# Optimization experiments

Measured on AMD Instinct MI355X. Metric: run time of the kernel, lower is better.

## Reference

```python
import jax, jax.numpy as jnp
import numpy as np

H, NH, NL, FF, W, CMAX, V, L, G = 768, 12, 6, 3072, 256, 32, 50272, 4096, 64
DH = H // NH
SCALE = 1.0 / np.sqrt(DH)

def _ln(x, s, b, eps=1e-5):
    m = jnp.mean(x, -1, keepdims=True)
    v = jnp.mean((x - m) ** 2, -1, keepdims=True)
    return (x - m) * jax.lax.rsqrt(v + eps) * s + b

def _heads(x, B, Lx):
    return x.reshape(B, Lx, NH, DH).transpose(0, 2, 1, 3)  # [B,NH,L,DH]

def _layer(x, p, am, gpos, is_glob):
    (Wq, bq, Wk, bk, Wv, bv, Wqg, bqg, Wkg, bkg, Wvg, bvg, Wo, bo,
     ln1s, ln1b, W1, b1, W2, b2, ln2s, ln2b) = p
    B, Lx, _ = x.shape
    Nb = Lx // W
    q = _heads(x @ Wq + bq, B, Lx)
    k = _heads(x @ Wk + bk, B, Lx)
    v = _heads(x @ Wv + bv, B, Lx)
    qb = q.reshape(B, NH, Nb, W, DH)
    def ctx(t):  # gather 3 adjacent key/value blocks per query block
        tb = t.reshape(B, NH, Nb, W, DH)
        tp = jnp.pad(tb, ((0, 0), (0, 0), (1, 1), (0, 0), (0, 0)))
        return jnp.stack([tp[:, :, i:i + Nb] for i in range(3)], axis=3).reshape(B, NH, Nb, 3 * W, DH)
    k_ctx, v_ctx = ctx(k), ctx(v)
    s_loc = jnp.einsum('bhnqd,bhnkd->bhnqk', qb, k_ctx) * SCALE  # [B,NH,Nb,W,3W]
    rel = jnp.arange(3 * W)[None, :] - W - jnp.arange(W)[:, None]  # [W,3W]
    band = jnp.abs(rel) <= W
    pos = jnp.arange(Nb)[:, None] * W + jnp.arange(3 * W)[None, :] - W  # abs key pos [Nb,3W]
    inb = (pos >= 0) & (pos < Lx)
    safe = jnp.clip(pos, 0, Lx - 1)
    key_ok = inb & (~is_glob[safe]) & am[:, safe]  # [B,Nb,3W]; global keys handled separately
    mask = key_ok[:, None, :, None, :] & band[None, None, None, :, :]
    s_loc = jnp.where(mask, s_loc, -1e9)
    # every token also attends to the G global tokens (global K/V projections)
    kg = _heads(x @ Wkg + bkg, B, Lx)
    vg = _heads(x @ Wvg + bvg, B, Lx)
    kgs, vgs = kg[:, :, gpos], vg[:, :, gpos]  # [B,NH,G,DH]
    s_glb = jnp.einsum('bhnqd,bhgd->bhnqg', qb, kgs) * SCALE
    attn = jax.nn.softmax(jnp.concatenate([s_loc, s_glb], -1), axis=-1)
    a_loc, a_glb = attn[..., :3 * W], attn[..., 3 * W:]
    out = jnp.einsum('bhnqk,bhnkd->bhnqd', a_loc, v_ctx) + jnp.einsum('bhnqg,bhgd->bhnqd', a_glb, vgs)
    out = out.reshape(B, NH, Lx, DH)
    # global query rows: full attention over all positions, overwrite outputs
    qg = _heads(x @ Wqg + bqg, B, Lx)[:, :, gpos]  # [B,NH,G,DH]
    s_full = jnp.einsum('bhgd,bhld->bhgl', qg, kg) * SCALE
    s_full = jnp.where(am[:, None, None, :], s_full, -1e9)
    og = jnp.einsum('bhgl,bhld->bhgd', jax.nn.softmax(s_full, -1), vg)
    out = out.at[:, :, gpos].set(og)
    out = out.transpose(0, 2, 1, 3).reshape(B, Lx, H)
    x = _ln(x + out @ Wo + bo, ln1s, ln1b)
    h = jax.nn.gelu(x @ W1 + b1, approximate=False)
    x = _ln(x + h @ W2 + b2, ln2s, ln2b)
    return x

def _forward(floats, input_ids, attention_mask, global_positions, cand_token_id):
    (emb_tok, emb_pos, lnes, lneb,
     Wq, bq, Wk, bk, Wv, bv, Wqg, bqg, Wkg, bkg, Wvg, bvg, Wo, bo,
     ln1_s, ln1_b, W1, b1, W2, b2, ln2_s, ln2_b, Wh1, bh1, Wh2, bh2) = floats
    B, Lx = input_ids.shape
    x = _ln(emb_tok[input_ids] + emb_pos[None, :Lx], lnes, lneb)
    is_glob = jnp.zeros(Lx, bool).at[global_positions].set(True)
    layers = (Wq, bq, Wk, bk, Wv, bv, Wqg, bqg, Wkg, bkg, Wvg, bvg, Wo, bo,
              ln1_s, ln1_b, W1, b1, W2, b2, ln2_s, ln2_b)
    def step(xc, p):
        return _layer(xc, p, attention_mask, global_positions, is_glob), None
    x, _ = jax.lax.scan(step, x, layers)
    # ListwiseRankingHead: gather hidden states at [CAND] marker positions
    cand_mask = input_ids == cand_token_id
    order = jnp.argsort(jnp.where(cand_mask, 0, 1).astype(jnp.int32), axis=1)  # stable
    positions = order[:, :CMAX]
    valid = jnp.take_along_axis(cand_mask, positions, axis=1)
    g = jnp.take_along_axis(x, positions[..., None], axis=1)  # [B,CMAX,H]
    h = jax.nn.gelu(g @ Wh1 + bh1, approximate=False)  # dropout is eval no-op
    logits = (h @ Wh2 + bh2).squeeze(-1)
    return logits, valid

def setup_inputs() -> dict:
    key = jax.random.key(0)
    ks = iter(jax.random.split(key, 64))
    r = lambda shape: jax.random.normal(next(ks), shape, jnp.float32) * 0.02
    B, CAND = 1, 50265
    d = {
        'emb_tok': r((V, H)), 'emb_pos': r((L, H)),
        'ln_emb_s': jnp.ones((H,), jnp.float32), 'ln_emb_b': jnp.zeros((H,), jnp.float32),
        'Wq': r((NL, H, H)), 'bq': jnp.zeros((NL, H), jnp.float32),
        'Wk': r((NL, H, H)), 'bk': jnp.zeros((NL, H), jnp.float32),
        'Wv': r((NL, H, H)), 'bv': jnp.zeros((NL, H), jnp.float32),
        'Wqg': r((NL, H, H)), 'bqg': jnp.zeros((NL, H), jnp.float32),
        'Wkg': r((NL, H, H)), 'bkg': jnp.zeros((NL, H), jnp.float32),
        'Wvg': r((NL, H, H)), 'bvg': jnp.zeros((NL, H), jnp.float32),
        'Wo': r((NL, H, H)), 'bo': jnp.zeros((NL, H), jnp.float32),
        'ln1_s': jnp.ones((NL, H), jnp.float32), 'ln1_b': jnp.zeros((NL, H), jnp.float32),
        'W1': r((NL, H, FF)), 'b1': jnp.zeros((NL, FF), jnp.float32),
        'W2': r((NL, FF, H)), 'b2': jnp.zeros((NL, H), jnp.float32),
        'ln2_s': jnp.ones((NL, H), jnp.float32), 'ln2_b': jnp.zeros((NL, H), jnp.float32),
        'Wh1': r((H, H // 2)), 'bh1': jnp.zeros((H // 2,), jnp.float32),
        'Wh2': r((H // 2, 1)), 'bh2': jnp.zeros((1,), jnp.float32),
    }
    input_ids = jax.random.randint(next(ks), (B, L), 0, CAND, dtype=jnp.int32)
    cand_pos = 256 + 128 * jnp.arange(30)  # 30 [CAND] markers
    input_ids = input_ids.at[:, cand_pos].set(CAND)
    d['input_ids'] = input_ids
    d['attention_mask'] = jnp.ones((B, L), jnp.bool_)
    d['global_positions'] = jnp.concatenate([jnp.arange(34), cand_pos]).astype(jnp.int32)  # CLS+query+markers
    d['cand_token_id'] = CAND
    return d

def reference(emb_tok, emb_pos, ln_emb_s, ln_emb_b, Wq, bq, Wk, bk, Wv, bv,
              Wqg, bqg, Wkg, bkg, Wvg, bvg, Wo, bo, ln1_s, ln1_b,
              W1, b1, W2, b2, ln2_s, ln2_b, Wh1, bh1, Wh2, bh2,
              input_ids, attention_mask, global_positions, cand_token_id):
    floats = (emb_tok, emb_pos, ln_emb_s, ln_emb_b, Wq, bq, Wk, bk, Wv, bv,
              Wqg, bqg, Wkg, bkg, Wvg, bvg, Wo, bo, ln1_s, ln1_b,
              W1, b1, W2, b2, ln2_s, ln2_b, Wh1, bh1, Wh2, bh2)
    return _forward(floats, input_ids, attention_mask, global_positions, cand_token_id)
```

## Files before the change

kernel.cpp:

```cpp
#include <hip/hip_runtime.h>
#include <hip/hip_bf16.h>
#include <math.h>

#define H 768
#define NH 12
#define DH 64
#define NL 6
#define FF 3072
#define LL 4096
#define GG 64
#define NCMAX 32

#define MATSZ (H * H)
#define OFF_QG ((size_t)5 * MATSZ)
#define OFF_O  ((size_t)6 * MATSZ)
#define OFF_W1 ((size_t)7 * MATSZ)
#define OFF_W2 (OFF_W1 + (size_t)H * FF)
#define WT_ELEMS (OFF_W2 + (size_t)FF * H)

typedef unsigned short u16;
typedef __attribute__((ext_vector_type(8))) unsigned short us8;
typedef __attribute__((ext_vector_type(4))) unsigned short us4;
typedef __attribute__((ext_vector_type(8))) __bf16 bf16x8;
typedef __attribute__((ext_vector_type(4))) float f32x4;
// ... 207 lines not shown
      int n = chunk * 8 + ml;
      gld16(Bt + (size_t)(n0 + n) * K + k0 + ((k8 ^ (n & 7)) * 8),
            &lsB[chunk * 512 + lane * 8]);
    }
    __syncthreads();
    #pragma unroll
    for (int kk = 0; kk < 2; ++kk) {
      bf16x8 fa[4], fb[4];
      int k8r = kk * 4 + kgr;
      #pragma unroll
      for (int i = 0; i < 4; ++i) {
        int mr = wm + i * 16 + cl;
        fa[i] = __builtin_bit_cast(bf16x8,
            *reinterpret_cast<const us8*>(&lsA[mr * 64 + ((k8r ^ (mr & 7)) * 8)]));
        int nr = wn + i * 16 + cl;
        fb[i] = __builtin_bit_cast(bf16x8,
            *reinterpret_cast<const us8*>(&lsB[nr * 64 + ((k8r ^ (nr & 7)) * 8)]));
      }
      #pragma unroll
      for (int i = 0; i < 4; ++i)
        #pragma unroll
        for (int j = 0; j < 4; ++j)
          acc[i][j] = __builtin_amdgcn_mfma_f32_16x16x32_bf16(fa[i], fb[j], acc[i][j], 0, 0, 0);
    }
    __syncthreads();
  }
}

template<int ACT>
__global__ __launch_bounds__(256) void gemm_bias_k(
    const u16* __restrict__ A, const u16* __restrict__ Bt, const float* __restrict__ bias,
    u16* __restrict__ outB, int M, int N, int K)
{
  __shared__ u16 lsA[128 * 64];
  __shared__ u16 lsB[128 * 64];
  int bx, by;
  tswz(bx, by);
  int m0 = by * 128, n0 = bx * 128;
  f32x4 zero4 = {0.f, 0.f, 0.f, 0.f};
  f32x4 acc[4][4];
  #pragma unroll
  for (int i = 0; i < 4; ++i)
    #pragma unroll
    for (int j = 0; j < 4; ++j) acc[i][j] = zero4;
  gemm_loop(A, Bt, K, m0, n0, 0, K, lsA, lsB, acc);
  int lane = threadIdx.x & 63, w = threadIdx.x >> 6;
  int cl = lane & 15, kgr = lane >> 4;
  int wm = (w >> 1) * 64, wn = (w & 1) * 64;
  #pragma unroll
  for (int j = 0; j < 4; ++j) {
    int n = n0 + wn + j * 16 + cl;
    float bv = bias[n];
    #pragma unroll
    for (int i = 0; i < 4; ++i) {
      #pragma unroll
      for (int r = 0; r < 4; ++r) {
        int m = m0 + wm + i * 16 + kgr * 4 + r;
        if (m < M) {
          float vv = acc[i][j][r] + bv;
          if (ACT == 1) vv = geluf(vv);
          outB[(size_t)m * N + n] = f2bf(vv);
        }
      }
    }
  }
}

__global__ __launch_bounds__(256) void gemm_part_k(
    const u16* __restrict__ A, const u16* __restrict__ Bt, float* __restrict__ part,
    int M, int N, int K)
{
  __shared__ u16 lsA[128 * 64];
  __shared__ u16 lsB[128 * 64];
  int bx, by;
  tswz(bx, by);
  int m0 = by * 128, n0 = bx * 128;
  int z = blockIdx.z, ns = gridDim.z;
  int ks = K / ns;
  f32x4 zero4 = {0.f, 0.f, 0.f, 0.f};
  f32x4 acc[4][4];
  #pragma unroll
  for (int i = 0; i < 4; ++i)
    #pragma unroll
    for (int j = 0; j < 4; ++j) acc[i][j] = zero4;
  gemm_loop(A, Bt, K, m0, n0, z * ks, (z + 1) * ks, lsA, lsB, acc);
  int lane = threadIdx.x & 63, w = threadIdx.x >> 6;
  int cl = lane & 15, kgr = lane >> 4;
  int wm = (w >> 1) * 64, wn = (w & 1) * 64;
  float* po = part + (size_t)z * LL * H;
  #pragma unroll
  for (int j = 0; j < 4; ++j) {
    int n = n0 + wn + j * 16 + cl;
    #pragma unroll
    for (int i = 0; i < 4; ++i) {
      #pragma unroll
      for (int r = 0; r < 4; ++r) {
        int m = m0 + wm + i * 16 + kgr * 4 + r;
        po[(size_t)m * N + n] = acc[i][j][r];
      }
    }
  }
}

__global__ __launch_bounds__(256) void gemm_qkv_k(
    const u16* __restrict__ A, const u16* __restrict__ Ag, const u16* __restrict__ wt,
    const float* c0, const float* c1, const float* c2, const float* c3, const float* c4,
    const float* c5,
    u16* o0, u16* o1, u16* o2, u16* o3, u16* o4, u16* o5)
{
  __shared__ u16 lsA[128 * 64];
  __shared__ u16 lsB[128 * 64];
  int z = blockIdx.z;
  int bx, by;
  tswz(bx, by);
  if (z == 5 && by != 0) return;
  const u16* Bt = wt + (size_t)z * MATSZ;
  const float* bias = z == 0 ? c0 : z == 1 ? c1 : z == 2 ? c2 : z == 3 ? c3 : z == 4 ? c4 : c5;
  u16* outB = z == 0 ? o0 : z == 1 ? o1 : z == 2 ? o2 : z == 3 ? o3 : z == 4 ? o4 : o5;
  const u16* Ap = (z == 5) ? Ag : A;
  int M = (z == 5) ? GG : LL;
  int m0 = by * 128, n0 = bx * 128;
  f32x4 zero4 = {0.f, 0.f, 0.f, 0.f};
  f32x4 acc[4][4];
  #pragma unroll
  for (int i = 0; i < 4; ++i)
    #pragma unroll
    for (int j = 0; j < 4; ++j) acc[i][j] = zero4;
  gemm_loop(Ap, Bt, H, m0, n0, 0, H, lsA, lsB, acc);
  int lane = threadIdx.x & 63, w = threadIdx.x >> 6;
  int cl = lane & 15, kgr = lane >> 4;
  int wm = (w >> 1) * 64, wn = (w & 1) * 64;
  #pragma unroll
  for (int j = 0; j < 4; ++j) {
    int n = n0 + wn + j * 16 + cl;
    float bv = bias[n];
    #pragma unroll
    for (int i = 0; i < 4; ++i) {
      #pragma unroll
      for (int r = 0; r < 4; ++r) {
        int m = m0 + wm + i * 16 + kgr * 4 + r;
        if (m < M) outB[(size_t)m * H + n] = f2bf(acc[i][j][r] + bv);
      }
    }
  }
}

__global__ __launch_bounds__(256) void attn_local_k(
    const u16* __restrict__ q, const u16* __restrict__ k, const u16* __restrict__ v,
    const u16* __restrict__ kgp, const u16* __restrict__ vgp,
    const int* __restrict__ gpos, const unsigned char* __restrict__ isg,
    u16* __restrict__ out)
{
  int h = blockIdx.x;
  int q0 = blockIdx.y * 64;
  int nb = q0 >> 8;
  int cs = (nb - 1) * 256;
  int cstart = (q0 >> 6) & 3;
  int t = threadIdx.x;
  int w = t >> 6, lane = t & 63;
  int cl = lane & 15, g = lane >> 4;
  __shared__ u16 sKb[2][64 * 64];
  __shared__ u16 sVtb[2][64 * 64];
  __shared__ u16 sP[64 * 64];
  __shared__ unsigned char sOkb[2][64];
  us8 z8 = {0, 0, 0, 0, 0, 0, 0, 0};
  f32x4 zero4 = {0.f, 0.f, 0.f, 0.f};

  int qrow = q0 + w * 16 + cl;
  bf16x8 qa[2];
  #pragma unroll
  for (int ks = 0; ks < 2; ++ks)
    qa[ks] = __builtin_bit_cast(bf16x8, *reinterpret_cast<const us8*>(
        &q[(size_t)qrow * H + h * 64 + ks * 32 + g * 8]));

  f32x4 O[4];
  #pragma unroll
  for (int dt = 0; dt < 4; ++dt) O[dt] = zero4;
  float mrow[4], lrow[4];
  #pragma unroll
  for (int r = 0; r < 4; ++r) { mrow[r] = -1e30f; lrow[r] = 0.f; }

  auto stage = [&](int ci, int buf) {
    bool isLocal = (ci < 9);
    int kbase = cs + (cstart + ci) * 64;
    #pragma unroll
    for (int it = 0; it < 2; ++it) {
      int idx = it * 256 + t;
      int key = idx >> 3, d8 = idx & 7;
      int pos;
      if (isLocal) {
        pos = kbase + key;
        pos = pos < 0 ? 0 : (pos >= LL ? LL - 1 : pos);
      } else {
        pos = gpos[key];
        pos = pos < 0 ? 0 : (pos >= LL ? LL - 1 : pos);
      }
      const u16* src = (isLocal ? k : kgp) + (size_t)pos * H + h * 64 + ((d8 ^ (key & 7)) * 8);
      gld16(src, &sKb[buf][idx * 8]);
    }
    #pragma unroll
    for (int it = 0; it < 2; ++it) {
      int idx = t + it * 256;
      int key = idx >> 3, d8 = idx & 7;
      us8 val = z8;
      if (isLocal) {
        int pos = kbase + key;
        if (pos >= 0 && pos < LL)
          val = *reinterpret_cast<const us8*>(&v[(size_t)pos * H + h * 64 + d8 * 8]);
      } else {
        int pos = gpos[key];
        if (pos < 0) pos = 0;
        if (pos >= LL) pos = LL - 1;
        val = *reinterpret_cast<const us8*>(&vgp[(size_t)pos * H + h * 64 + d8 * 8]);
      }
      int k8 = key >> 3, klow = key & 7;
      int kswz = (k8 ^ d8) * 8 + klow;
      #pragma unroll
      for (int u = 0; u < 8; ++u)
        sVtb[buf][(d8 * 8 + u) * 64 + kswz] = val[u];
    }
    if (t < 64) {
      int ok = 1;
      if (isLocal) {
        int pos = kbase + t;
        ok = (pos >= 0 && pos < LL) ? (isg[pos] ? 0 : 1) : 0;
      }
      sOkb[buf][t] = (unsigned char)ok;
    }
  };

  stage(0, 0);
  int buf = 0;
  for (int ci = 0; ci < 10; ++ci) {
    __syncthreads();
    if (ci < 9) stage(ci + 1, buf ^ 1);
    bool isLocal = (ci < 9);
    int kbase = cs + (cstart + ci) * 64;
    const u16* sK = sKb[buf];
    const u16* sVt = sVtb[buf];
    const unsigned char* sOk = sOkb[buf];

    f32x4 S[4];
    #pragma unroll
    for (int T = 0; T < 4; ++T) {
      S[T] = zero4;
      int key = T * 16 + cl;
      #pragma unroll
      for (int ks = 0; ks < 2; ++ks) {
        bf16x8 kf = __builtin_bit_cast(bf16x8, *reinterpret_cast<const us8*>(
            &sK[key * 64 + (((ks * 4 + g) ^ (key & 7)) * 8)]));
        S[T] = __builtin_amdgcn_mfma_f32_16x16x32_bf16(qa[ks], kf, S[T], 0, 0, 0);
      }
    }
    #pragma unroll
    for (int T = 0; T < 4; ++T) {
      int key = T * 16 + cl;
      int okk = sOk[key];
      int pos = kbase + key;
      #pragma unroll
      for (int r = 0; r < 4; ++r) {
        int qp = q0 + w * 16 + g * 4 + r;
        int d = pos - qp;
        bool ok = okk && (!isLocal || (d >= -256 && d <= 256));
        S[T][r] = ok ? S[T][r] * 0.125f : -1e9f;
      }
    }
    float cm[4];
    #pragma unroll
    for (int r = 0; r < 4; ++r) {
      cm[r] = fmaxf(fmaxf(S[0][r], S[1][r]), fmaxf(S[2][r], S[3][r]));
      cm[r] = fmaxf(cm[r], __shfl_xor(cm[r], 1));
      cm[r] = fmaxf(cm[r], __shfl_xor(cm[r], 2));
      cm[r] = fmaxf(cm[r], __shfl_xor(cm[r], 4));
      cm[r] = fmaxf(cm[r], __shfl_xor(cm[r], 8));
    }
    float sc[4];
    #pragma unroll
    for (int r = 0; r < 4; ++r) {
      float mn = fmaxf(mrow[r], cm[r]);
      sc[r] = __expf(mrow[r] - mn);
      mrow[r] = mn;
    }
    float rs[4] = {0.f, 0.f, 0.f, 0.f};
    #pragma unroll
    for (int T = 0; T < 4; ++T) {
      int key = T * 16 + cl;
      #pragma unroll
      for (int r = 0; r < 4; ++r) {
        float sv = S[T][r];
        float pv = sv > -1e8f ? __expf(sv - mrow[r]) : 0.f;
        rs[r] += pv;
        int qloc = w * 16 + g * 4 + r;
        int k8s = (key >> 3) ^ (qloc & 7);
        sP[qloc * 64 + k8s * 8 + (key & 7)] = f2bf(pv);
      }
    }
    #pragma unroll
    for (int r = 0; r < 4; ++r) {
      rs[r] += __shfl_xor(rs[r], 1);
      rs[r] += __shfl_xor(rs[r], 2);
      rs[r] += __shfl_xor(rs[r], 4);
      rs[r] += __shfl_xor(rs[r], 8);
      lrow[r] = lrow[r] * sc[r] + rs[r];
    }
    #pragma unroll
    for (int dt = 0; dt < 4; ++dt)
      #pragma unroll
      for (int r = 0; r < 4; ++r) O[dt][r] *= sc[r];
    int prow = w * 16 + cl;
    #pragma unroll
    for (int ks = 0; ks < 2; ++ks) {
      bf16x8 pf = __builtin_bit_cast(bf16x8, *reinterpret_cast<const us8*>(
          &sP[prow * 64 + (((ks * 4 + g) ^ (prow & 7)) * 8)]));
      #pragma unroll
      for (int dt = 0; dt < 4; ++dt) {
        int dim = dt * 16 + cl;
        int k8s = (ks * 4 + g) ^ ((dim >> 3) & 7);
        bf16x8 vf = __builtin_bit_cast(bf16x8, *reinterpret_cast<const us8*>(
            &sVt[dim * 64 + k8s * 8]));
        O[dt] = __builtin_amdgcn_mfma_f32_16x16x32_bf16(pf, vf, O[dt], 0, 0, 0);
      }
    }
    buf ^= 1;
  }
  #pragma unroll
  for (int r = 0; r < 4; ++r) {
    float inv = 1.f / lrow[r];
    int qp = q0 + w * 16 + g * 4 + r;
    #pragma unroll
    for (int dt = 0; dt < 4; ++dt)
      out[(size_t)qp * H + h * 64 + dt * 16 + cl] = f2bf(O[dt][r] * inv);
  }
}

__global__ __launch_bounds__(256) void ag_score_k(
    const u16* __restrict__ qg, const u16* __restrict__ kg, float* __restrict__ sbuf)
{
  int h = blockIdx.x;
  int kc0 = blockIdx.y * 128;
  int t = threadIdx.x;
  int w = t >> 6, lane = t & 63;
  int cl = lane & 15, g = lane >> 4;
  __shared__ u16 sK[128 * 64];
  #pragma unroll
  for (int it = 0; it < 4; ++it) {
    int idx = it * 256 + t;
    int key = idx >> 3, d8 = idx & 7;
    gld16(kg + (size_t)(kc0 + key) * H + h * 64 + ((d8 ^ (key & 7)) * 8), &sK[idx * 8]);
  }
  int qrow = w * 16 + cl;
  bf16x8 qa[2];
  #pragma unroll
  for (int ks = 0; ks < 2; ++ks)
    qa[ks] = __builtin_bit_cast(bf16x8, *reinterpret_cast<const us8*>(
        &qg[(size_t)qrow * H + h * 64 + ks * 32 + g * 8]));
  __syncthreads();
  f32x4 zero4 = {0.f, 0.f, 0.f, 0.f};
  #pragma unroll
  for (int j = 0; j < 8; ++j) {
    f32x4 S = zero4;
    int key = j * 16 + cl;
    #pragma unroll
    for (int ks = 0; ks < 2; ++ks) {
      bf16x8 kf = __builtin_bit_cast(bf16x8, *reinterpret_cast<const us8*>(
          &sK[key * 64 + (((ks * 4 + g) ^ (key & 7)) * 8)]));
      S = __builtin_amdgcn_mfma_f32_16x16x32_bf16(qa[ks], kf, S, 0, 0, 0);
    }
    #pragma unroll
    for (int r = 0; r < 4; ++r) {
      int grow = w * 16 + g * 4 + r;
      sbuf[((size_t)(h * 64 + grow)) * 4096 + kc0 + key] = S[r] * 0.125f;
    }
  }
}

__global__ __launch_bounds__(256) void ag_soft_k(float* __restrict__ sbuf)
{
  int row = blockIdx.x, t = threadIdx.x;
  float* base = sbuf + (size_t)row * 4096;
  u16* pb = (u16*)(sbuf) + (size_t)row * 8192;
  __shared__ float red[4];
  f32x4 rv[4];
  #pragma unroll
  for (int it = 0; it < 4; ++it)
    rv[it] = *reinterpret_cast<const f32x4*>(base + it * 1024 + t * 4);
  float m = -1e30f;
  #pragma unroll
  for (int it = 0; it < 4; ++it)
    #pragma unroll
    for (int u = 0; u < 4; ++u) m = fmaxf(m, rv[it][u]);
  m = wredmax(m);
  if ((t & 63) == 0) red[t >> 6] = m;
  __syncthreads();
  m = fmaxf(fmaxf(red[0], red[1]), fmaxf(red[2], red[3]));
  __syncthreads();
  float s = 0.f;
  #pragma unroll
  for (int it = 0; it < 4; ++it)
    #pragma unroll
    for (int u = 0; u < 4; ++u) {
      float e = __expf(rv[it][u] - m);
      rv[it][u] = e;
      s += e;
    }
  s = wredsum(s);
  if ((t & 63) == 0) red[t >> 6] = s;
  __syncthreads();
  float inv = 1.f / (red[0] + red[1] + red[2] + red[3]);
  #pragma unroll
  for (int it = 0; it < 4; ++it) {
    us4 o;
    #pragma unroll
    for (int u = 0; u < 4; ++u) o[u] = f2bf(rv[it][u] * inv);
    *reinterpret_cast<us4*>(pb + it * 1024 + t * 4) = o;
  }
}

__global__ __launch_bounds__(256) void ag_pv_k(
    const float* __restrict__ sbuf, const u16* __restrict__ vg, float* __restrict__ obuf)
{
  int h = blockIdx.x;
  int kb0 = blockIdx.y * 256;
  int t = threadIdx.x;
  int w = t >> 6, lane = t & 63;
  int cl = lane & 15, g = lane >> 4;
  __shared__ u16 sVt[64 * 64];
  f32x4 zero4 = {0.f, 0.f, 0.f, 0.f};
  f32x4 O[4];
  #pragma unroll
  for (int dt = 0; dt < 4; ++dt) O[dt] = zero4;
  const u16* pb = (const u16*)(sbuf);
  int prow = w * 16 + cl;
  size_t pbase = (size_t)(h * 64 + prow) * 8192;

  for (int cc = 0; cc < 4; ++cc) {
    int kc = kb0 + cc * 64;
    #pragma unroll
    for (int it = 0; it < 2; ++it) {
      int idx = t + it * 256;
      int key = idx >> 3, d8 = idx & 7;
      us8 val = *reinterpret_cast<const us8*>(&vg[(size_t)(kc + key) * H + h * 64 + d8 * 8]);
      int k8 = key >> 3, klow = key & 7;
      int kswz = (k8 ^ d8) * 8 + klow;
      #pragma unroll
      for (int u = 0; u < 8; ++u)
        sVt[(d8 * 8 + u) * 64 + kswz] = val[u];
    }
    __syncthreads();
    #pragma unroll
    for (int ks = 0; ks < 2; ++ks) {
      bf16x8 pf = __builtin_bit_cast(bf16x8, *reinterpret_cast<const us8*>(
          pb + pbase + kc + (ks * 4 + g) * 8));
      #pragma unroll
      for (int dt = 0; dt < 4; ++dt) {
        int dim = dt * 16 + cl;
        int k8s = (ks * 4 + g) ^ ((dim >> 3) & 7);
        bf16x8 vf = __builtin_bit_cast(bf16x8, *reinterpret_cast<const us8*>(
            &sVt[dim * 64 + k8s * 8]));
        O[dt] = __builtin_amdgcn_mfma_f32_16x16x32_bf16(pf, vf, O[dt], 0, 0, 0);
      }
    }
    __syncthreads();
  }
  #pragma unroll
  for (int r = 0; r < 4; ++r) {
    int grow = w * 16 + g * 4 + r;
    #pragma unroll
    for (int dt = 0; dt < 4; ++dt)
      atomicAdd(&obuf[((size_t)h * 64 + grow) * 64 + dt * 16 + cl], O[dt][r]);
  }
}

__global__ __launch_bounds__(256) void ag_write_k(
    float* __restrict__ obuf, const int* __restrict__ gpos, u16* __restrict__ out)
{
  int g = blockIdx.x, t = threadIdx.x;
  int gp = gpos[g];
  if (gp < 0) gp = 0;
  if (gp >= LL) gp = LL - 1;
  #pragma unroll
  for (int e = 0; e < 3; ++e) {
    int c = t + e * 256;
    int h = c >> 6, d = c & 63;
    size_t idx = ((size_t)h * 64 + g) * 64 + d;
    out[(size_t)gp * H + c] = f2bf(obuf[idx]);
    obuf[idx] = 0.f;
  }
}

__global__ void setup_k(const int* __restrict__ gpos, unsigned char* __restrict__ isg,
                        int* __restrict__ ginv,
                        const int* __restrict__ ids, const int* __restrict__ candp,
                        int* __restrict__ posb, float* __restrict__ outp) {
  int t = threadIdx.x;
  for (int i = t; i < LL; i += 256) { isg[i] = 0; ginv[i] = -1; }
  __syncthreads();
  if (t < GG) {
    int gp = gpos[t];
    if (gp >= 0 && gp < LL) { isg[gp] = 1; ginv[gp] = t; }
  }
  int cand = candp[0];
  __shared__ int cnt[257];
  int base = t * 16, c0 = 0;
  for (int u = 0; u < 16; ++u) c0 += (ids[base + u] == cand) ? 1 : 0;
  cnt[t + 1] = c0;
  __syncthreads();
  if (t == 0) {
    cnt[0] = 0;
    for (int i2 = 1; i2 <= 256; ++i2) cnt[i2] += cnt[i2 - 1];
  }
  __syncthreads();
  int ncand = cnt[256];
  int cr = cnt[t];
  for (int u = 0; u < 16; ++u) {
    int i2 = base + u;
    bool isC = (ids[i2] == cand);
    if (isC) {
      if (cr < NCMAX) posb[cr] = i2;
      cr++;
    } else {
      int nc = i2 - cr;
      int slot = ncand + nc;
      if (slot < NCMAX && nc >= 0) posb[slot] = i2;
    }
  }
  if (t < NCMAX) outp[NCMAX + t] = (t < ncand) ? 1.f : 0.f;
}

__global__ __launch_bounds__(256) void head_k(
    const float* __restrict__ x, const int* __restrict__ posb,
    const float* __restrict__ Wh1, const float* __restrict__ bh1,
    const float* __restrict__ Wh2, const float* __restrict__ bh2, float* __restrict__ outp) {
  int s = blockIdx.x, t = threadIdx.x;
  int p = posb[s];
  if (p < 0) p = 0;
  if (p >= LL) p = LL - 1;
  __shared__ float sx[H];
  __shared__ float sh[384];
  __shared__ float red[4];
  #pragma unroll
  for (int e = 0; e < 3; ++e) sx[t + e * 256] = x[(size_t)p * H + t + e * 256];
  __syncthreads();
  for (int j = t; j < 384; j += 256) {
    float a = bh1[j];
    for (int c = 0; c < H; ++c) a += sx[c] * Wh1[(size_t)c * 384 + j];
    sh[j] = geluf(a);
  }
  __syncthreads();
  float part = 0.f;
  for (int j = t; j < 384; j += 256) part += sh[j] * Wh2[j];
  part = wredsum(part);
  if ((t & 63) == 0) red[t >> 6] = part;
  __syncthreads();
  if (t == 0) {
    float tot = red[0] + red[1] + red[2] + red[3] + bh2[0];
    outp[s] = tot;
  }
}

extern "C" void kernel_launch(void* const* d_in, const int* in_sizes, int n_in,
                              void* d_out, int out_size, void* d_ws, size_t ws_size,
                              hipStream_t stream) {
  const float* emb_tok = (const float*)d_in[0];
  const float* emb_pos = (const float*)d_in[1];
  const float* lnes = (const float*)d_in[2];
  const float* lneb = (const float*)d_in[3];
  const float* Wq = (const float*)d_in[4];
  const float* bq = (const float*)d_in[5];
  const float* Wk = (const float*)d_in[6];
  const float* bk = (const float*)d_in[7];
  const float* Wv = (const float*)d_in[8];
  const float* bv = (const float*)d_in[9];
  const float* Wqg = (const float*)d_in[10];
  const float* bqg = (const float*)d_in[11];
  const float* Wkg = (const float*)d_in[12];
  const float* bkg = (const float*)d_in[13];
  const float* Wvg = (const float*)d_in[14];
  const float* bvg = (const float*)d_in[15];
  const float* Wo = (const float*)d_in[16];
  const float* bo = (const float*)d_in[17];
  const float* ln1s = (const float*)d_in[18];
  const float* ln1b = (const float*)d_in[19];
  const float* W1 = (const float*)d_in[20];
  const float* b1 = (const float*)d_in[21];
  const float* W2 = (const float*)d_in[22];
  const float* b2 = (const float*)d_in[23];
  const float* ln2s = (const float*)d_in[24];
  const float* ln2b = (const float*)d_in[25];
  const float* Wh1 = (const float*)d_in[26];
  const float* bh1 = (const float*)d_in[27];
  const float* Wh2 = (const float*)d_in[28];
  const float* bh2 = (const float*)d_in[29];
  const int* ids = (const int*)d_in[30];
  int i_gpos = 32, i_cand = 33;
  if (!(n_in >= 34 && in_sizes[32] == GG)) {
    if (n_in >= 33 && in_sizes[31] == GG) { i_gpos = 31; i_cand = 32; }
  }
  const int* gpos = (const int*)d_in[i_gpos];
  const int* cand = (const int*)d_in[i_cand];
  float* outp = (float*)d_out;

  char* p = (char*)d_ws;
  auto alloc = [&](size_t bytes) {
    char* r = p;
    p += (bytes + 255) & ~(size_t)255;
    return r;
  };
  float* x = (float*)alloc((size_t)LL * H * 4);
  u16* xb = (u16*)alloc((size_t)LL * H * 2);
  u16* qb = (u16*)alloc((size_t)LL * H * 2);
  u16* kb = (u16*)alloc((size_t)LL * H * 2);
  u16* vb = (u16*)alloc((size_t)LL * H * 2);
  u16* kgb = (u16*)alloc((size_t)LL * H * 2);
  u16* vgb = (u16*)alloc((size_t)LL * H * 2);
  u16* ob = (u16*)alloc((size_t)LL * H * 2);
  u16* qgb = (u16*)alloc((size_t)GG * H * 2);
  u16* xgb = (u16*)alloc((size_t)128 * H * 2);
  unsigned char* isg = (unsigned char*)alloc(LL);
  int* ginv = (int*)alloc(LL * 4);
  int* posb = (int*)alloc(64 * 4);
  u16* wtb = (u16*)alloc((size_t)NL * WT_ELEMS * 2);
  float* sbuf = (float*)alloc((size_t)NH * 64 * 4096 * 4);
  float* obuf = (float*)alloc((size_t)NH * 64 * 64 * 4);
  float* partb = (float*)alloc((size_t)4 * LL * H * 4);
  u16* hb = qb;

  hipMemsetAsync(obuf, 0, (size_t)NH * 64 * 64 * 4, stream);

  setup_k<<<1, 256, 0, stream>>>(gpos, isg, ginv, ids, cand, posb, outp);
  conv_all_k<<<dim3(1080, NL), 256, 0, stream>>>(Wq, Wk, Wv, Wkg, Wvg, Wqg, Wo, W1, W2, wtb);
  embed_ln_k<<<LL, 256, 0, stream>>>(emb_tok, emb_pos, ids, lnes, lneb, ginv, x, xb, xgb);

  dim3 gP2(H / 128, LL / 128, 2);
  dim3 gP4(H / 128, LL / 128, 4);
  dim3 gF(FF / 128, LL / 128);
  dim3 gQKV(H / 128, LL / 128, 6);
  for (int l = 0; l < NL; ++l) {
    u16* wt = wtb + (size_t)l * WT_ELEMS;
    gemm_qkv_k<<<gQKV, 256, 0, stream>>>(xb, xgb, wt,
        bq + l * H, bk + l * H, bv + l * H, bkg + l * H, bvg + l * H, bqg + l * H,
        qb, kb, vb, kgb, vgb, qgb);
    attn_local_k<<<dim3(NH, LL / 64), 256, 0, stream>>>(qb, kb, vb, kgb, vgb, gpos, isg, ob);
    ag_score_k<<<dim3(NH, LL / 128), 256, 0, stream>>>(qgb, kgb, sbuf);
    ag_soft_k<<<NH * 64, 256, 0, stream>>>(sbuf);
    ag_pv_k<<<dim3(NH, LL / 256), 256, 0, stream>>>(sbuf, vgb, obuf);
    ag_write_k<<<GG, 256, 0, stream>>>(obuf, gpos, ob);
    gemm_part_k<<<gP2, 256, 0, stream>>>(ob, wt + OFF_O, partb, LL, H, H);
    ln_res2_k<2><<<LL, 256, 0, stream>>>(x, partb, bo + l * H, ln1s + l * H, ln1b + l * H, ginv, xb, xgb);
    gemm_bias_k<1><<<gF, 256, 0, stream>>>(xb, wt + OFF_W1, b1 + l * FF, hb, LL, FF, H);
    gemm_part_k<<<gP4, 256, 0, stream>>>(hb, wt + OFF_W2, partb, LL, H, FF);
    ln_res2_k<4><<<LL, 256, 0, stream>>>(x, partb, b2 + l * H, ln2s + l * H, ln2b + l * H, ginv, xb, xgb);
  }
  head_k<<<NCMAX, 256, 0, stream>>>(x, posb, Wh1, bh1, Wh2, bh2, outp);
}
```

Baseline: 1.466 ms.

## Process 128 queries per attention block and fuse global-attn writeback into PV

The local attention kernel now handles two 64-query groups per block, so each staged K/V chunk is reused by both. That needs 10 local chunks instead of 9 to cover the wider window, and the grid is halved. Separately, the global-query write kernel is removed: the last PV block per head, found with an atomic counter, reads and clears the accumulated output and scatters it. This cuts K/V reloads and one launch, at the cost of more registers, lower occupancy, extra masked chunk work, and atomic/fence overhead.

New measurement: 1.670 ms. 13.9% more time.

```diff
diff --git a/kernel.cpp b/kernel.cpp
--- a/kernel.cpp
+++ b/kernel.cpp
@@ -383,7 +383,7 @@
     u16* __restrict__ out)
 {
   int h = blockIdx.x;
-  int q0 = blockIdx.y * 64;
+  int q0 = blockIdx.y * 128;
   int nb = q0 >> 8;
   int cs = (nb - 1) * 256;
   int cstart = (q0 >> 6) & 3;
@@ -392,27 +392,33 @@
   int cl = lane & 15, g = lane >> 4;
   __shared__ u16 sKb[2][64 * 64];
   __shared__ u16 sVtb[2][64 * 64];
-  __shared__ u16 sP[64 * 64];
+  __shared__ u16 sP[128 * 64];
   __shared__ unsigned char sOkb[2][64];
   us8 z8 = {0, 0, 0, 0, 0, 0, 0, 0};
   f32x4 zero4 = {0.f, 0.f, 0.f, 0.f};
 
-  int qrow = q0 + w * 16 + cl;
-  bf16x8 qa[2];
-  #pragma unroll
-  for (int ks = 0; ks < 2; ++ks)
-    qa[ks] = __builtin_bit_cast(bf16x8, *reinterpret_cast<const us8*>(
-        &q[(size_t)qrow * H + h * 64 + ks * 32 + g * 8]));
-
-  f32x4 O[4];
-  #pragma unroll
-  for (int dt = 0; dt < 4; ++dt) O[dt] = zero4;
-  float mrow[4], lrow[4];
-  #pragma unroll
-  for (int r = 0; r < 4; ++r) { mrow[r] = -1e30f; lrow[r] = 0.f; }
+  bf16x8 qa[2][2];
+  #pragma unroll
+  for (int grp = 0; grp < 2; ++grp) {
+    int qrow = q0 + grp * 64 + w * 16 + cl;
+    #pragma unroll
+    for (int ks = 0; ks < 2; ++ks)
+      qa[grp][ks] = __builtin_bit_cast(bf16x8, *reinterpret_cast<const us8*>(
+          &q[(size_t)qrow * H + h * 64 + ks * 32 + g * 8]));
+  }
+
+  f32x4 O[2][4];
+  float mrow[2][4], lrow[2][4];
+  #pragma unroll
+  for (int grp = 0; grp < 2; ++grp) {
+    #pragma unroll
+    for (int dt = 0; dt < 4; ++dt) O[grp][dt] = zero4;
+    #pragma unroll
+    for (int r = 0; r < 4; ++r) { mrow[grp][r] = -1e30f; lrow[grp][r] = 0.f; }
+  }
 
   auto stage = [&](int ci, int buf) {
-    bool isLocal = (ci < 9);
+    bool isLocal = (ci < 10);
     int kbase = cs + (cstart + ci) * 64;
     #pragma unroll
     for (int it = 0; it < 2; ++it) {
@@ -462,87 +468,234 @@
 
   stage(0, 0);
   int buf = 0;
-  for (int ci = 0; ci < 10; ++ci) {
+  for (int ci = 0; ci < 11; ++ci) {
     __syncthreads();
-    if (ci < 9) stage(ci + 1, buf ^ 1);
-    bool isLocal = (ci < 9);
+    if (ci < 10) stage(ci + 1, buf ^ 1);
+    bool isLocal = (ci < 10);
     int kbase = cs + (cstart + ci) * 64;
     const u16* sK = sKb[buf];
     const u16* sVt = sVtb[buf];
     const unsigned char* sOk = sOkb[buf];
 
-    f32x4 S[4];
-    #pragma unroll
-    for (int T = 0; T < 4; ++T) {
-      S[T] = zero4;
-      int key = T * 16 + cl;
+    #pragma unroll
+    for (int grp = 0; grp < 2; ++grp) {
+      f32x4 S[4];
+      #pragma unroll
+      for (int T = 0; T < 4; ++T) {
+        S[T] = zero4;
+        int key = T * 16 + cl;
+        #pragma unroll
+        for (int ks = 0; ks < 2; ++ks) {
+          bf16x8 kf = __builtin_bit_cast(bf16x8, *reinterpret_cast<const us8*>(
+              &sK[key * 64 + (((ks * 4 + g) ^ (key & 7)) * 8)]));
+          S[T] = __builtin_amdgcn_mfma_f32_16x16x32_bf16(qa[grp][ks], kf, S[T], 0, 0, 0);
+        }
+      }
+      #pragma unroll
+      for (int T = 0; T < 4; ++T) {
+        int key = T * 16 + cl;
+        int okk = sOk[key];
+        int pos = kbase + key;
+        #pragma unroll
+        for (int r = 0; r < 4; ++r) {
+          int qp = q0 + grp * 64 + w * 16 + g * 4 + r;
+          int d = pos - qp;
+          bool ok = okk && (!isLocal || (d >= -256 && d <= 256));
+          S[T][r] = ok ? S[T][r] * 0.125f : -1e9f;
+        }
+      }
+      float cm[4];
+      #pragma unroll
+      for (int r = 0; r < 4; ++r) {
+        cm[r] = fmaxf(fmaxf(S[0][r], S[1][r]), fmaxf(S[2][r], S[3][r]));
+        cm[r] = fmaxf(cm[r], __shfl_xor(cm[r], 1));
+        cm[r] = fmaxf(cm[r], __shfl_xor(cm[r], 2));
+        cm[r] = fmaxf(cm[r], __shfl_xor(cm[r], 4));
+        cm[r] = fmaxf(cm[r], __shfl_xor(cm[r], 8));
+      }
+      float sc[4];
+      #pragma unroll
+      for (int r = 0; r < 4; ++r) {
+        float mn = fmaxf(mrow[grp][r], cm[r]);
+        sc[r] = __expf(mrow[grp][r] - mn);
+        mrow[grp][r] = mn;
+      }
+      float rs[4] = {0.f, 0.f, 0.f, 0.f};
+      #pragma unroll
+      for (int T = 0; T < 4; ++T) {
+        int key = T * 16 + cl;
+        #pragma unroll
+        for (int r = 0; r < 4; ++r) {
+          float sv = S[T][r];
+          float pv = sv > -1e8f ? __expf(sv - mrow[grp][r]) : 0.f;
+          rs[r] += pv;
+          int qloc = grp * 64 + w * 16 + g * 4 + r;
+          int k8s = (key >> 3) ^ (qloc & 7);
+          sP[qloc * 64 + k8s * 8 + (key & 7)] = f2bf(pv);
+        }
+      }
+      #pragma unroll
+      for (int r = 0; r < 4; ++r) {
+        rs[r] += __shfl_xor(rs[r], 1);
+        rs[r] += __shfl_xor(rs[r], 2);
+        rs[r] += __shfl_xor(rs[r], 4);
+        rs[r] += __shfl_xor(rs[r], 8);
+        lrow[grp][r] = lrow[grp][r] * sc[r] + rs[r];
+      }
+      #pragma unroll
+      for (int dt = 0; dt < 4; ++dt)
+        #pragma unroll
+        for (int r = 0; r < 4; ++r) O[grp][dt][r] *= sc[r];
+      int prow = grp * 64 + w * 16 + cl;
       #pragma unroll
       for (int ks = 0; ks < 2; ++ks) {
-        bf16x8 kf = __builtin_bit_cast(bf16x8, *reinterpret_cast<const us8*>(
-            &sK[key * 64 + (((ks * 4 + g) ^ (key & 7)) * 8)]));
-        S[T] = __builtin_amdgcn_mfma_f32_16x16x32_bf16(qa[ks], kf, S[T], 0, 0, 0);
-      }
-    }
-    #pragma unroll
-    for (int T = 0; T < 4; ++T) {
-      int key = T * 16 + cl;
-      int okk = sOk[key];
-      int pos = kbase + key;
-      #pragma unroll
-      for (int r = 0; r < 4; ++r) {
-        int qp = q0 + w * 16 + g * 4 + r;
-        int d = pos - qp;
-        bool ok = okk && (!isLocal || (d >= -256 && d <= 256));
-        S[T][r] = ok ? S[T][r] * 0.125f : -1e9f;
-      }
-    }
-    float cm[4];
+        bf16x8 pf = __builtin_bit_cast(bf16x8, *reinterpret_cast<const us8*>(
+            &sP[prow * 64 + (((ks * 4 + g) ^ (prow & 7)) * 8)]));
+        #pragma unroll
+        for (int dt = 0; dt < 4; ++dt) {
+          int dim = dt * 16 + cl;
+          int k8s = (ks * 4 + g) ^ ((dim >> 3) & 7);
+          bf16x8 vf = __builtin_bit_cast(bf16x8, *reinterpret_cast<const us8*>(
+              &sVt[dim * 64 + k8s * 8]));
+          O[grp][dt] = __builtin_amdgcn_mfma_f32_16x16x32_bf16(pf, vf, O[grp][dt], 0, 0, 0);
+        }
+      }
+    }
+    buf ^= 1;
+  }
+  #pragma unroll
+  for (int grp = 0; grp < 2; ++grp) {
     #pragma unroll
     for (int r = 0; r < 4; ++r) {
-      cm[r] = fmaxf(fmaxf(S[0][r], S[1][r]), fmaxf(S[2][r], S[3][r]));
-      cm[r] = fmaxf(cm[r], __shfl_xor(cm[r], 1));
-      cm[r] = fmaxf(cm[r], __shfl_xor(cm[r], 2));
-      cm[r] = fmaxf(cm[r], __shfl_xor(cm[r], 4));
-      cm[r] = fmaxf(cm[r], __shfl_xor(cm[r], 8));
-    }
-    float sc[4];
+      float inv = 1.f / lrow[grp][r];
+      int qp = q0 + grp * 64 + w * 16 + g * 4 + r;
+      #pragma unroll
+      for (int dt = 0; dt < 4; ++dt)
+        out[(size_t)qp * H + h * 64 + dt * 16 + cl] = f2bf(O[grp][dt][r] * inv);
+    }
+  }
+}
+
+__global__ __launch_bounds__(256) void ag_score_k(
+    const u16* __restrict__ qg, const u16* __restrict__ kg, float* __restrict__ sbuf)
+{
+  int h = blockIdx.x;
+  int kc0 = blockIdx.y * 128;
+  int t = threadIdx.x;
+  int w = t >> 6, lane = t & 63;
+  int cl = lane & 15, g = lane >> 4;
+  __shared__ u16 sK[128 * 64];
+  #pragma unroll
+  for (int it = 0; it < 4; ++it) {
+    int idx = it * 256 + t;
+    int key = idx >> 3, d8 = idx & 7;
+    gld16(kg + (size_t)(kc0 + key) * H + h * 64 + ((d8 ^ (key & 7)) * 8), &sK[idx * 8]);
+  }
+  int qrow = w * 16 + cl;
+  bf16x8 qa[2];
+  #pragma unroll
+  for (int ks = 0; ks < 2; ++ks)
+    qa[ks] = __builtin_bit_cast(bf16x8, *reinterpret_cast<const us8*>(
+        &qg[(size_t)qrow * H + h * 64 + ks * 32 + g * 8]));
+  __syncthreads();
+  f32x4 zero4 = {0.f, 0.f, 0.f, 0.f};
+  #pragma unroll
+  for (int j = 0; j < 8; ++j) {
+    f32x4 S = zero4;
+    int key = j * 16 + cl;
+    #pragma unroll
+    for (int ks = 0; ks < 2; ++ks) {
+      bf16x8 kf = __builtin_bit_cast(bf16x8, *reinterpret_cast<const us8*>(
+          &sK[key * 64 + (((ks * 4 + g) ^ (key & 7)) * 8)]));
+      S = __builtin_amdgcn_mfma_f32_16x16x32_bf16(qa[ks], kf, S, 0, 0, 0);
+    }
     #pragma unroll
     for (int r = 0; r < 4; ++r) {
-      float mn = fmaxf(mrow[r], cm[r]);
-      sc[r] = __expf(mrow[r] - mn);
-      mrow[r] = mn;
-    }
-    float rs[4] = {0.f, 0.f, 0.f, 0.f};
-    #pragma unroll
-    for (int T = 0; T < 4; ++T) {
-      int key = T * 16 + cl;
-      #pragma unroll
-      for (int r = 0; r < 4; ++r) {
-        float sv = S[T][r];
-        float pv = sv > -1e8f ? __expf(sv - mrow[r]) : 0.f;
-        rs[r] += pv;
-        int qloc = w * 16 + g * 4 + r;
-        int k8s = (key >> 3) ^ (qloc & 7);
-        sP[qloc * 64 + k8s * 8 + (key & 7)] = f2bf(pv);
-      }
-    }
-    #pragma unroll
-    for (int r = 0; r < 4; ++r) {
-      rs[r] += __shfl_xor(rs[r], 1);
-      rs[r] += __shfl_xor(rs[r], 2);
-      rs[r] += __shfl_xor(rs[r], 4);
-      rs[r] += __shfl_xor(rs[r], 8);
-      lrow[r] = lrow[r] * sc[r] + rs[r];
-    }
-    #pragma unroll
-    for (int dt = 0; dt < 4; ++dt)
-      #pragma unroll
-      for (int r = 0; r < 4; ++r) O[dt][r] *= sc[r];
-    int prow = w * 16 + cl;
+      int grow = w * 16 + g * 4 + r;
+      sbuf[((size_t)(h * 64 + grow)) * 4096 + kc0 + key] = S[r] * 0.125f;
+    }
+  }
+}
+
+__global__ __launch_bounds__(256) void ag_soft_k(float* __restrict__ sbuf)
+{
+  int row = blockIdx.x, t = threadIdx.x;
+  float* base = sbuf + (size_t)row * 4096;
+  u16* pb = (u16*)(sbuf) + (size_t)row * 8192;
+  __shared__ float red[4];
+  f32x4 rv[4];
+  #pragma unroll
+  for (int it = 0; it < 4; ++it)
+    rv[it] = *reinterpret_cast<const f32x4*>(base + it * 1024 + t * 4);
+  float m = -1e30f;
+  #pragma unroll
+  for (int it = 0; it < 4; ++it)
+    #pragma unroll
+    for (int u = 0; u < 4; ++u) m = fmaxf(m, rv[it][u]);
+  m = wredmax(m);
+  if ((t & 63) == 0) red[t >> 6] = m;
+  __syncthreads();
+  m = fmaxf(fmaxf(red[0], red[1]), fmaxf(red[2], red[3]));
+  __syncthreads();
+  float s = 0.f;
+  #pragma unroll
+  for (int it = 0; it < 4; ++it)
+    #pragma unroll
+    for (int u = 0; u < 4; ++u) {
+      float e = __expf(rv[it][u] - m);
+      rv[it][u] = e;
+      s += e;
+    }
+  s = wredsum(s);
+  if ((t & 63) == 0) red[t >> 6] = s;
+  __syncthreads();
+  float inv = 1.f / (red[0] + red[1] + red[2] + red[3]);
+  #pragma unroll
+  for (int it = 0; it < 4; ++it) {
+    us4 o;
+    #pragma unroll
+    for (int u = 0; u < 4; ++u) o[u] = f2bf(rv[it][u] * inv);
+    *reinterpret_cast<us4*>(pb + it * 1024 + t * 4) = o;
+  }
+}
+
+__global__ __launch_bounds__(256) void ag_pv_k(
+    const float* __restrict__ sbuf, const u16* __restrict__ vg, float* __restrict__ obuf,
+    const int* __restrict__ gpos, u16* __restrict__ out, int* __restrict__ cnt)
+{
+  int h = blockIdx.x;
+  int kb0 = blockIdx.y * 256;
+  int t = threadIdx.x;
+  int w = t >> 6, lane = t & 63;
+  int cl = lane & 15, g = lane >> 4;
+  __shared__ u16 sVt[64 * 64];
+  __shared__ int lastFlag;
+  f32x4 zero4 = {0.f, 0.f, 0.f, 0.f};
+  f32x4 O[4];
+  #pragma unroll
+  for (int dt = 0; dt < 4; ++dt) O[dt] = zero4;
+  const u16* pb = (const u16*)(sbuf);
+  int prow = w * 16 + cl;
+  size_t pbase = (size_t)(h * 64 + prow) * 8192;
+
+  for (int cc = 0; cc < 4; ++cc) {
+    int kc = kb0 + cc * 64;
+    #pragma unroll
+    for (int it = 0; it < 2; ++it) {
+      int idx = t + it * 256;
+      int key = idx >> 3, d8 = idx & 7;
+      us8 val = *reinterpret_cast<const us8*>(&vg[(size_t)(kc + key) * H + h * 64 + d8 * 8]);
+      int k8 = key >> 3, klow = key & 7;
+      int kswz = (k8 ^ d8) * 8 + klow;
+      #pragma unroll
+      for (int u = 0; u < 8; ++u)
+        sVt[(d8 * 8 + u) * 64 + kswz] = val[u];
+    }
+    __syncthreads();
     #pragma unroll
     for (int ks = 0; ks < 2; ++ks) {
       bf16x8 pf = __builtin_bit_cast(bf16x8, *reinterpret_cast<const us8*>(
-          &sP[prow * 64 + (((ks * 4 + g) ^ (prow & 7)) * 8)]));
+          pb + pbase + kc + (ks * 4 + g) * 8));
       #pragma unroll
       for (int dt = 0; dt < 4; ++dt) {
         int dim = dt * 16 + cl;
@@ -552,145 +705,6 @@
         O[dt] = __builtin_amdgcn_mfma_f32_16x16x32_bf16(pf, vf, O[dt], 0, 0, 0);
       }
     }
-    buf ^= 1;
-  }
-  #pragma unroll
-  for (int r = 0; r < 4; ++r) {
-    float inv = 1.f / lrow[r];
-    int qp = q0 + w * 16 + g * 4 + r;
-    #pragma unroll
-    for (int dt = 0; dt < 4; ++dt)
-      out[(size_t)qp * H + h * 64 + dt * 16 + cl] = f2bf(O[dt][r] * inv);
-  }
-}
-
-__global__ __launch_bounds__(256) void ag_score_k(
-    const u16* __restrict__ qg, const u16* __restrict__ kg, float* __restrict__ sbuf)
-{
-  int h = blockIdx.x;
-  int kc0 = blockIdx.y * 128;
-  int t = threadIdx.x;
-  int w = t >> 6, lane = t & 63;
-  int cl = lane & 15, g = lane >> 4;
-  __shared__ u16 sK[128 * 64];
-  #pragma unroll
-  for (int it = 0; it < 4; ++it) {
-    int idx = it * 256 + t;
-    int key = idx >> 3, d8 = idx & 7;
-    gld16(kg + (size_t)(kc0 + key) * H + h * 64 + ((d8 ^ (key & 7)) * 8), &sK[idx * 8]);
-  }
-  int qrow = w * 16 + cl;
-  bf16x8 qa[2];
-  #pragma unroll
-  for (int ks = 0; ks < 2; ++ks)
-    qa[ks] = __builtin_bit_cast(bf16x8, *reinterpret_cast<const us8*>(
-        &qg[(size_t)qrow * H + h * 64 + ks * 32 + g * 8]));
-  __syncthreads();
-  f32x4 zero4 = {0.f, 0.f, 0.f, 0.f};
-  #pragma unroll
-  for (int j = 0; j < 8; ++j) {
-    f32x4 S = zero4;
-    int key = j * 16 + cl;
-    #pragma unroll
-    for (int ks = 0; ks < 2; ++ks) {
-      bf16x8 kf = __builtin_bit_cast(bf16x8, *reinterpret_cast<const us8*>(
-          &sK[key * 64 + (((ks * 4 + g) ^ (key & 7)) * 8)]));
-      S = __builtin_amdgcn_mfma_f32_16x16x32_bf16(qa[ks], kf, S, 0, 0, 0);
-    }
-    #pragma unroll
-    for (int r = 0; r < 4; ++r) {
-      int grow = w * 16 + g * 4 + r;
-      sbuf[((size_t)(h * 64 + grow)) * 4096 + kc0 + key] = S[r] * 0.125f;
-    }
-  }
-}
-
-__global__ __launch_bounds__(256) void ag_soft_k(float* __restrict__ sbuf)
-{
-  int row = blockIdx.x, t = threadIdx.x;
-  float* base = sbuf + (size_t)row * 4096;
-  u16* pb = (u16*)(sbuf) + (size_t)row * 8192;
-  __shared__ float red[4];
-  f32x4 rv[4];
-  #pragma unroll
-  for (int it = 0; it < 4; ++it)
-    rv[it] = *reinterpret_cast<const f32x4*>(base + it * 1024 + t * 4);
-  float m = -1e30f;
-  #pragma unroll
-  for (int it = 0; it < 4; ++it)
-    #pragma unroll
-    for (int u = 0; u < 4; ++u) m = fmaxf(m, rv[it][u]);
-  m = wredmax(m);
-  if ((t & 63) == 0) red[t >> 6] = m;
-  __syncthreads();
-  m = fmaxf(fmaxf(red[0], red[1]), fmaxf(red[2], red[3]));
-  __syncthreads();
-  float s = 0.f;
-  #pragma unroll
-  for (int it = 0; it < 4; ++it)
-    #pragma unroll
-    for (int u = 0; u < 4; ++u) {
-      float e = __expf(rv[it][u] - m);
-      rv[it][u] = e;
-      s += e;
-    }
-  s = wredsum(s);
-  if ((t & 63) == 0) red[t >> 6] = s;
-  __syncthreads();
-  float inv = 1.f / (red[0] + red[1] + red[2] + red[3]);
-  #pragma unroll
-  for (int it = 0; it < 4; ++it) {
-    us4 o;
-    #pragma unroll
-    for (int u = 0; u < 4; ++u) o[u] = f2bf(rv[it][u] * inv);
-    *reinterpret_cast<us4*>(pb + it * 1024 + t * 4) = o;
-  }
-}
-
-__global__ __launch_bounds__(256) void ag_pv_k(
-    const float* __restrict__ sbuf, const u16* __restrict__ vg, float* __restrict__ obuf)
-{
-  int h = blockIdx.x;
-  int kb0 = blockIdx.y * 256;
-  int t = threadIdx.x;
-  int w = t >> 6, lane = t & 63;
-  int cl = lane & 15, g = lane >> 4;
-  __shared__ u16 sVt[64 * 64];
-  f32x4 zero4 = {0.f, 0.f, 0.f, 0.f};
-  f32x4 O[4];
-  #pragma unroll
-  for (int dt = 0; dt < 4; ++dt) O[dt] = zero4;
-  const u16* pb = (const u16*)(sbuf);
-  int prow = w * 16 + cl;
-  size_t pbase = (size_t)(h * 64 + prow) * 8192;
-
-  for (int cc = 0; cc < 4; ++cc) {
-    int kc = kb0 + cc * 64;
-    #pragma unroll
-    for (int it = 0; it < 2; ++it) {
-      int idx = t + it * 256;
-      int key = idx >> 3, d8 = idx & 7;
-      us8 val = *reinterpret_cast<const us8*>(&vg[(size_t)(kc + key) * H + h * 64 + d8 * 8]);
-      int k8 = key >> 3, klow = key & 7;
-      int kswz = (k8 ^ d8) * 8 + klow;
-      #pragma unroll
-      for (int u = 0; u < 8; ++u)
-        sVt[(d8 * 8 + u) * 64 + kswz] = val[u];
-    }
-    __syncthreads();
-    #pragma unroll
-    for (int ks = 0; ks < 2; ++ks) {
-      bf16x8 pf = __builtin_bit_cast(bf16x8, *reinterpret_cast<const us8*>(
-          pb + pbase + kc + (ks * 4 + g) * 8));
-      #pragma unroll
-      for (int dt = 0; dt < 4; ++dt) {
-        int dim = dt * 16 + cl;
-        int k8s = (ks * 4 + g) ^ ((dim >> 3) & 7);
-        bf16x8 vf = __builtin_bit_cast(bf16x8, *reinterpret_cast<const us8*>(
-            &sVt[dim * 64 + k8s * 8]));
-        O[dt] = __builtin_amdgcn_mfma_f32_16x16x32_bf16(pf, vf, O[dt], 0, 0, 0);
-      }
-    }
     __syncthreads();
   }
   #pragma unroll
@@ -700,49 +714,54 @@
     for (int dt = 0; dt < 4; ++dt)
       atomicAdd(&obuf[((size_t)h * 64 + grow) * 64 + dt * 16 + cl], O[dt][r]);
   }
-}
-
-__global__ __launch_bounds__(256) void ag_write_k(
-    float* __restrict__ obuf, const int* __restrict__ gpos, u16* __restrict__ out)
-{
-  int g = blockIdx.x, t = threadIdx.x;
-  int gp = gpos[g];
-  if (gp < 0) gp = 0;
-  if (gp >= LL) gp = LL - 1;
-  #pragma unroll
-  for (int e = 0; e < 3; ++e) {
-    int c = t + e * 256;
-    int h = c >> 6, d = c & 63;
-    size_t idx = ((size_t)h * 64 + g) * 64 + d;
-    out[(size_t)gp * H + c] = f2bf(obuf[idx]);
-    obuf[idx] = 0.f;
+  __threadfence();
+  if (t == 0) {
+    int old = atomicAdd(&cnt[h], 1);
+    lastFlag = (old == (int)gridDim.y - 1) ? 1 : 0;
+    if (lastFlag) cnt[h] = 0;
+  }
+  __syncthreads();
+  if (lastFlag) {
+    __threadfence();
+    #pragma unroll
+    for (int e = 0; e < 16; ++e) {
+      int idx2 = t + e * 256;
+      int gq = idx2 >> 6, d = idx2 & 63;
+      int gp = gpos[gq];
+      if (gp < 0) gp = 0;
+      if (gp >= LL) gp = LL - 1;
+      size_t oidx = ((size_t)h * 64 + gq) * 64 + d;
+      float val = atomicExch(&obuf[oidx], 0.f);
+      out[(size_t)gp * H + h * 64 + d] = f2bf(val);
+    }
   }
 }
 
 __global__ void setup_k(const int* __restrict__ gpos, unsigned char* __restrict__ isg,
-                        int* __restrict__ ginv,
+                        int* __restrict__ ginv, int* __restrict__ cnt,
                         const int* __restrict__ ids, const int* __restrict__ candp,
                         int* __restrict__ posb, float* __restrict__ outp) {
   int t = threadIdx.x;
   for (int i = t; i < LL; i += 256) { isg[i] = 0; ginv[i] = -1; }
+  if (t < NH) cnt[t] = 0;
   __syncthreads();
   if (t < GG) {
     int gp = gpos[t];
     if (gp >= 0 && gp < LL) { isg[gp] = 1; ginv[gp] = t; }
   }
   int cand = candp[0];
-  __shared__ int cnt[257];
+  __shared__ int cntr[257];
   int base = t * 16, c0 = 0;
   for (int u = 0; u < 16; ++u) c0 += (ids[base + u] == cand) ? 1 : 0;
-  cnt[t + 1] = c0;
+  cntr[t + 1] = c0;
   __syncthreads();
   if (t == 0) {
-    cnt[0] = 0;
-    for (int i2 = 1; i2 <= 256; ++i2) cnt[i2] += cnt[i2 - 1];
-  }
-  __syncthreads();
-  int ncand = cnt[256];
-  int cr = cnt[t];
+    cntr[0] = 0;
+    for (int i2 = 1; i2 <= 256; ++i2) cntr[i2] += cntr[i2 - 1];
+  }
+  __syncthreads();
+  int ncand = cntr[256];
+  int cr = cntr[t];
   for (int u = 0; u < 16; ++u) {
     int i2 = base + u;
     bool isC = (ids[i2] == cand);
@@ -850,6 +869,7 @@
   unsigned char* isg = (unsigned char*)alloc(LL);
   int* ginv = (int*)alloc(LL * 4);
   int* posb = (int*)alloc(64 * 4);
+  int* cntb = (int*)alloc(NH * 4);
   u16* wtb = (u16*)alloc((size_t)NL * WT_ELEMS * 2);
   float* sbuf = (float*)alloc((size_t)NH * 64 * 4096 * 4);
   float* obuf = (float*)alloc((size_t)NH * 64 * 64 * 4);
@@ -858,7 +878,7 @@
 
   hipMemsetAsync(obuf, 0, (size_t)NH * 64 * 64 * 4, stream);
 
-  setup_k<<<1, 256, 0, stream>>>(gpos, isg, ginv, ids, cand, posb, outp);
+  setup_k<<<1, 256, 0, stream>>>(gpos, isg, ginv, cntb, ids, cand, posb, outp);
   conv_all_k<<<dim3(1080, NL), 256, 0, stream>>>(Wq, Wk, Wv, Wkg, Wvg, Wqg, Wo, W1, W2, wtb);
   embed_ln_k<<<LL, 256, 0, stream>>>(emb_tok, emb_pos, ids, lnes, lneb, ginv, x, xb, xgb);
 
@@ -871,11 +891,10 @@
     gemm_qkv_k<<<gQKV, 256, 0, stream>>>(xb, xgb, wt,
         bq + l * H, bk + l * H, bv + l * H, bkg + l * H, bvg + l * H, bqg + l * H,
         qb, kb, vb, kgb, vgb, qgb);
-    attn_local_k<<<dim3(NH, LL / 64), 256, 0, stream>>>(qb, kb, vb, kgb, vgb, gpos, isg, ob);
+    attn_local_k<<<dim3(NH, LL / 128), 256, 0, stream>>>(qb, kb, vb, kgb, vgb, gpos, isg, ob);
     ag_score_k<<<dim3(NH, LL / 128), 256, 0, stream>>>(qgb, kgb, sbuf);
     ag_soft_k<<<NH * 64, 256, 0, stream>>>(sbuf);
-    ag_pv_k<<<dim3(NH, LL / 256), 256, 0, stream>>>(sbuf, vgb, obuf);
-    ag_write_k<<<GG, 256, 0, stream>>>(obuf, gpos, ob);
+    ag_pv_k<<<dim3(NH, LL / 256), 256, 0, stream>>>(sbuf, vgb, obuf, gpos, ob, cntb);
     gemm_part_k<<<gP2, 256, 0, stream>>>(ob, wt + OFF_O, partb, LL, H, H);
     ln_res2_k<2><<<LL, 256, 0, stream>>>(x, partb, bo + l * H, ln1s + l * H, ln1b + l * H, ginv, xb, xgb);
     gemm_bias_k<1><<<gF, 256, 0, stream>>>(xb, wt + OFF_W1, b1 + l * FF, hb, LL, FF, H);
```
